# Kernel tuning notes

Hardware: AMD Instinct MI355X
Metric: run time of the kernel (lower is better)

Reference implementation:

```python
import jax, jax.numpy as jnp
import numpy as np

EPS = 1e-8  # matches TMLoss(eps=1e-08)


def setup_inputs() -> dict:
    key = jax.random.key(0)
    k1, k2 = jax.random.split(key)
    b, n = 2048, 1024
    # pseudo protein coords: spread out like real structures (~tens of Angstroms)
    pred = jax.random.normal(k1, (b, n, 3), dtype=jnp.float32) * 10.0
    # native coords = pred + noise, arbitrarily rotated/translated is fine since we Kabsch-align
    actual = pred + jax.random.normal(k2, (b, n, 3), dtype=jnp.float32)
    return {"predicted_coords": pred, "actual_coords": actual}


def _kabsch_align(align_to, align_from):
    """Rigidly align align_from onto align_to (batched Kabsch). Shapes (b,n,3)."""
    mu_to = jnp.mean(align_to, axis=1, keepdims=True)
    mu_from = jnp.mean(align_from, axis=1, keepdims=True)
    p = align_to - mu_to      # (b,n,3) target, centered
    q = align_from - mu_from  # (b,n,3) mobile, centered
    # 3x3 cross-covariance M = q^T p; optimal R maximizes tr(R^T M)
    M = jnp.einsum('bni,bnj->bij', q, p)  # (b,3,3)
    U, S, Vt = jnp.linalg.svd(M)
    # proper-rotation (det=+1) correction on smallest singular direction
    d = jnp.sign(jnp.linalg.det(U) * jnp.linalg.det(Vt))  # (b,)
    ones = jnp.ones_like(d)
    D = jnp.stack([ones, ones, d], axis=-1)               # (b,3)
    R = jnp.einsum('bik,bk,bkj->bij', U, D, Vt)           # (b,3,3)
    aligned = jnp.einsum('bni,bij->bnj', q, R) + mu_to    # (b,n,3)
    return align_to, aligned


def _calc_tm(dev, reduce=True):
    """dev: (b,n) per-residue deviations -> TM-score."""
    n = dev.shape[-1]
    d0 = 1.24 * (n - 15.0) ** (1.0 / 3.0) - 1.8
    tm = jnp.mean(1.0 / (1.0 + (dev / d0) ** 2), axis=-1)  # (b,)
    return jnp.mean(tm) if reduce else tm


def reference(predicted_coords, actual_coords):
    # align=True path: Kabsch-align native onto prediction
    _, aligned_actual = _kabsch_align(predicted_coords, actual_coords)
    # per-residue deviation (eps added elementwise before norm, as in torch source)
    dev = jnp.linalg.norm(predicted_coords - aligned_actual + EPS, axis=-1)  # (b,n)
    return -_calc_tm(dev, reduce=True)
```

## Files before the change

### kernel.cpp

```cpp
#include <hip/hip_runtime.h>
#include <math.h>

#define NRES 1024
#define TM_EPS 1e-8f

__global__ __launch_bounds__(256, 2) void tm_fused(const float* __restrict__ pred,
                                                   const float* __restrict__ act,
                                                   float* __restrict__ out,
                                                   float scale, float inv_d02) {
    __shared__ float4 sh[6][256];
    __shared__ float red[4][15];
    __shared__ float rotsh[12];

    int b = blockIdx.x;
    int t = threadIdx.x;
    const float4* p4 = (const float4*)(pred + (size_t)b * NRES * 3);
    const float4* a4 = (const float4*)(act  + (size_t)b * NRES * 3);

    float4 pf0 = p4[3 * t + 0], pf1 = p4[3 * t + 1], pf2 = p4[3 * t + 2];
    float4 af0 = a4[3 * t + 0], af1 = a4[3 * t + 1], af2 = a4[3 * t + 2];
    sh[0][t] = pf0; sh[1][t] = pf1; sh[2][t] = pf2;
    sh[3][t] = af0; sh[4][t] = af1; sh[5][t] = af2;

    {
        float px[4] = {pf0.x, pf0.w, pf1.z, pf2.y};
        float py[4] = {pf0.y, pf1.x, pf1.w, pf2.z};
        float pz[4] = {pf0.z, pf1.y, pf2.x, pf2.w};
        float ax[4] = {af0.x, af0.w, af1.z, af2.y};
        float ay[4] = {af0.y, af1.x, af1.w, af2.z};
        float az[4] = {af0.z, af1.y, af2.x, af2.w};

        float acc[15];
#pragma unroll
        for (int i = 0; i < 15; i++) acc[i] = 0.f;
#pragma unroll
        for (int r = 0; r < 4; r++) {
            acc[0] += px[r]; acc[1] += py[r]; acc[2] += pz[r];
            acc[3] += ax[r]; acc[4] += ay[r]; acc[5] += az[r];
            acc[6]  += ax[r] * px[r]; acc[7]  += ax[r] * py[r]; acc[8]  += ax[r] * pz[r];
            acc[9]  += ay[r] * px[r]; acc[10] += ay[r] * py[r]; acc[11] += ay[r] * pz[r];
            acc[12] += az[r] * px[r]; acc[13] += az[r] * py[r]; acc[14] += az[r] * pz[r];
        }
#pragma unroll
        for (int off = 32; off > 0; off >>= 1) {
#pragma unroll
            for (int i = 0; i < 15; i++) acc[i] += __shfl_down(acc[i], off);
        }
        int wave = t >> 6, lane = t & 63;
        if (lane == 0) {
#pragma unroll
            for (int i = 0; i < 15; i++) red[wave][i] = acc[i];
        }
    }
    __syncthreads();

    if (t == 0) {
        float s[15];
#pragma unroll
        for (int i = 0; i < 15; i++) s[i] = red[0][i] + red[1][i] + red[2][i] + red[3][i];

        const double n = (double)NRES;
        double mp[3], mq[3];
#pragma unroll
        for (int i = 0; i < 3; i++) { mp[i] = (double)s[i] / n; mq[i] = (double)s[3 + i] / n; }
        double M[3][3];
#pragma unroll
        for (int i = 0; i < 3; i++)
#pragma unroll
            for (int j = 0; j < 3; j++)
                M[i][j] = (double)s[6 + i * 3 + j] - n * mq[i] * mp[j];

        double Sxx = M[0][0], Sxy = M[0][1], Sxz = M[0][2];
        double Syx = M[1][0], Syy = M[1][1], Syz = M[1][2];
        double Szx = M[2][0], Szy = M[2][1], Szz = M[2][2];
        double K[4][4];
        K[0][0] = Sxx + Syy + Szz; K[0][1] = Syz - Szy;        K[0][2] = Szx - Sxz;         K[0][3] = Sxy - Syx;
        K[1][0] = K[0][1];         K[1][1] = Sxx - Syy - Szz;  K[1][2] = Sxy + Syx;         K[1][3] = Szx + Sxz;
        K[2][0] = K[0][2];         K[2][1] = K[1][2];          K[2][2] = -Sxx + Syy - Szz;  K[2][3] = Syz + Szy;
        K[3][0] = K[0][3];         K[3][1] = K[1][3];          K[3][2] = K[2][3];           K[3][3] = -Sxx - Syy + Szz;

        double K2[4][4];
#pragma unroll
        for (int i = 0; i < 4; i++)
#pragma unroll
            for (int j = 0; j < 4; j++) {
                double acc = 0.0;
#pragma unroll
                for (int k = 0; k < 4; k++) acc += K[i][k] * K[k][j];
                K2[i][j] = acc;
            }
        double p2 = 0.0, p3 = 0.0, p4s = 0.0;
#pragma unroll
        for (int i = 0; i < 4; i++)
#pragma unroll
            for (int j = 0; j < 4; j++) {
                p2 += K[i][j] * K[i][j];
                p3 += K2[i][j] * K[i][j];
                p4s += K2[i][j] * K2[i][j];
            }
        double e2 = -0.5 * p2;
        double e3 = p3 / 3.0;
        double e4 = (0.5 * p2 * p2 - p4s) * 0.25;

        double lam = sqrt(p2);
#pragma unroll
        for (int it = 0; it < 14; it++) {
            double lam2 = lam * lam;
            double P  = lam2 * lam2 + e2 * lam2 - e3 * lam + e4;
            double Pp = 4.0 * lam * lam2 + 2.0 * e2 * lam - e3;
            lam -= P / Pp;
        }

        double Bm[4][4];
#pragma unroll
        for (int i = 0; i < 4; i++)
#pragma unroll
            for (int j = 0; j < 4; j++) Bm[i][j] = K[i][j] - ((i == j) ? lam : 0.0);

        double cand[4][4];
#pragma unroll
        for (int r = 0; r < 4; r++) {
            int rr[3]; int k = 0;
#pragma unroll
            for (int i = 0; i < 4; i++) if (i != r) rr[k++] = i;
#pragma unroll
            for (int c = 0; c < 4; c++) {
                int cc[3]; int m = 0;
#pragma unroll
                for (int j = 0; j < 4; j++) if (j != c) cc[m++] = j;
                double d =
                    Bm[rr[0]][cc[0]] * (Bm[rr[1]][cc[1]] * Bm[rr[2]][cc[2]] - Bm[rr[1]][cc[2]] * Bm[rr[2]][cc[1]])
                  - Bm[rr[0]][cc[1]] * (Bm[rr[1]][cc[0]] * Bm[rr[2]][cc[2]] - Bm[rr[1]][cc[2]] * Bm[rr[2]][cc[0]])
                  + Bm[rr[0]][cc[2]] * (Bm[rr[1]][cc[0]] * Bm[rr[2]][cc[1]] - Bm[rr[1]][cc[1]] * Bm[rr[2]][cc[0]]);
                cand[r][c] = (((r + c) & 1) ? -d : d);
            }
        }
        int bestr = 0;
        double bestn = -1.0;
#pragma unroll
        for (int r = 0; r < 4; r++) {
            double nn = cand[r][0] * cand[r][0] + cand[r][1] * cand[r][1] +
                        cand[r][2] * cand[r][2] + cand[r][3] * cand[r][3];
            if (nn > bestn) { bestn = nn; bestr = r; }
        }
        double w = cand[bestr][0], x = cand[bestr][1], y = cand[bestr][2], z = cand[bestr][3];
        double nrm = sqrt(w * w + x * x + y * y + z * z);
        w /= nrm; x /= nrm; y /= nrm; z /= nrm;

        double A[3][3];
        A[0][0] = 1.0 - 2.0 * (y * y + z * z); A[0][1] = 2.0 * (x * y - w * z);       A[0][2] = 2.0 * (x * z + w * y);
        A[1][0] = 2.0 * (x * y + w * z);       A[1][1] = 1.0 - 2.0 * (x * x + z * z); A[1][2] = 2.0 * (y * z - w * x);
        A[2][0] = 2.0 * (x * z - w * y);       A[2][1] = 2.0 * (y * z + w * x);       A[2][2] = 1.0 - 2.0 * (x * x + y * y);

#pragma unroll
        for (int i = 0; i < 3; i++)
#pragma unroll
            for (int j = 0; j < 3; j++) rotsh[i * 3 + j] = (float)A[i][j];
#pragma unroll
        for (int i = 0; i < 3; i++)
            rotsh[9 + i] = (float)(mp[i] - (A[i][0] * mq[0] + A[i][1] * mq[1] + A[i][2] * mq[2]));
    }
    __syncthreads();

    float A00 = rotsh[0], A01 = rotsh[1], A02 = rotsh[2];
    float A10 = rotsh[3], A11 = rotsh[4], A12 = rotsh[5];
    float A20 = rotsh[6], A21 = rotsh[7], A22 = rotsh[8];
    float t0 = rotsh[9], t1 = rotsh[10], t2 = rotsh[11];

    float4 qf0 = sh[0][t], qf1 = sh[1][t], qf2 = sh[2][t];
    float4 bf0 = sh[3][t], bf1 = sh[4][t], bf2 = sh[5][t];

    float px[4] = {qf0.x, qf0.w, qf1.z, qf2.y};
    float py[4] = {qf0.y, qf1.x, qf1.w, qf2.z};
    float pz[4] = {qf0.z, qf1.y, qf2.x, qf2.w};
    float ax[4] = {bf0.x, bf0.w, bf1.z, bf2.y};
    float ay[4] = {bf0.y, bf1.x, bf1.w, bf2.z};
    float az[4] = {bf0.z, bf1.y, bf2.x, bf2.w};

    float sc = 0.f;
#pragma unroll
    for (int r = 0; r < 4; r++) {
        float dx = px[r] - (A00 * ax[r] + A01 * ay[r] + A02 * az[r]) - t0 + TM_EPS;
        float dy = py[r] - (A10 * ax[r] + A11 * ay[r] + A12 * az[r]) - t1 + TM_EPS;
        float dz = pz[r] - (A20 * ax[r] + A21 * ay[r] + A22 * az[r]) - t2 + TM_EPS;
        float d2 = dx * dx + dy * dy + dz * dz;
        sc += 1.0f / (1.0f + d2 * inv_d02);
    }
#pragma unroll
    for (int off = 32; off > 0; off >>= 1) sc += __shfl_down(sc, off);

    __shared__ float red2[4];
    int wave = t >> 6, lane = t & 63;
    if (lane == 0) red2[wave] = sc;
    __syncthreads();
    if (t == 0) {
        float tot = red2[0] + red2[1] + red2[2] + red2[3];
        atomicAdd(out, -tot * scale);
    }
}

extern "C" void kernel_launch(void* const* d_in, const int* in_sizes, int n_in,
                              void* d_out, int out_size, void* d_ws, size_t ws_size,
                              hipStream_t stream) {
    const float* pred = (const float*)d_in[0];
    const float* act  = (const float*)d_in[1];
    float* out = (float*)d_out;
    int B = in_sizes[0] / (NRES * 3);

    hipMemsetAsync(d_out, 0, sizeof(float), stream);

    double d0 = 1.24 * cbrt((double)NRES - 15.0) - 1.8;
    float inv_d02 = (float)(1.0 / (d0 * d0));
    float scale = 1.0f / ((float)B * (float)NRES);
    tm_fused<<<B, 256, 0, stream>>>(pred, act, out, scale, inv_d02);
}
```

Measured before the change: 110.1 us.

## Keep coordinates in registers and compute the rotation solve in fp32

Coordinates now stay in registers across the rotation solve instead of being staged through a 24KB shared-memory buffer. The single-thread quaternion eigen-solve switches from double to float, with two fewer Newton iterations and a reciprocal sqrt for normalisation. Launch bounds go from 2 to 4 blocks per SIMD to raise occupancy. This targets the serial fp64 tail run by thread 0 and the LDS limit on occupancy. The risks are fp32 accuracy loss in the covariance and eigenvalue steps and register pressure from holding 24 floats live across the solve.

After: 106.7 us. 3.0% less time.

```diff
diff --git a/kernel.cpp b/kernel.cpp
--- a/kernel.cpp
+++ b/kernel.cpp
@@ -4,13 +4,13 @@
 #define NRES 1024
 #define TM_EPS 1e-8f
 
-__global__ __launch_bounds__(256, 2) void tm_fused(const float* __restrict__ pred,
+__global__ __launch_bounds__(256, 4) void tm_fused(const float* __restrict__ pred,
                                                    const float* __restrict__ act,
                                                    float* __restrict__ out,
                                                    float scale, float inv_d02) {
-    __shared__ float4 sh[6][256];
     __shared__ float red[4][15];
     __shared__ float rotsh[12];
+    __shared__ float red2[4];
 
     int b = blockIdx.x;
     int t = threadIdx.x;
@@ -19,17 +19,15 @@
 
     float4 pf0 = p4[3 * t + 0], pf1 = p4[3 * t + 1], pf2 = p4[3 * t + 2];
     float4 af0 = a4[3 * t + 0], af1 = a4[3 * t + 1], af2 = a4[3 * t + 2];
-    sh[0][t] = pf0; sh[1][t] = pf1; sh[2][t] = pf2;
-    sh[3][t] = af0; sh[4][t] = af1; sh[5][t] = af2;
+
+    float px[4] = {pf0.x, pf0.w, pf1.z, pf2.y};
+    float py[4] = {pf0.y, pf1.x, pf1.w, pf2.z};
+    float pz[4] = {pf0.z, pf1.y, pf2.x, pf2.w};
+    float ax[4] = {af0.x, af0.w, af1.z, af2.y};
+    float ay[4] = {af0.y, af1.x, af1.w, af2.z};
+    float az[4] = {af0.z, af1.y, af2.x, af2.w};
 
     {
-        float px[4] = {pf0.x, pf0.w, pf1.z, pf2.y};
-        float py[4] = {pf0.y, pf1.x, pf1.w, pf2.z};
-        float pz[4] = {pf0.z, pf1.y, pf2.x, pf2.w};
-        float ax[4] = {af0.x, af0.w, af1.z, af2.y};
-        float ay[4] = {af0.y, af1.x, af1.w, af2.z};
-        float az[4] = {af0.z, af1.y, af2.x, af2.w};
-
         float acc[15];
 #pragma unroll
         for (int i = 0; i < 15; i++) acc[i] = 0.f;
@@ -59,37 +57,37 @@
 #pragma unroll
         for (int i = 0; i < 15; i++) s[i] = red[0][i] + red[1][i] + red[2][i] + red[3][i];
 
-        const double n = (double)NRES;
-        double mp[3], mq[3];
-#pragma unroll
-        for (int i = 0; i < 3; i++) { mp[i] = (double)s[i] / n; mq[i] = (double)s[3 + i] / n; }
-        double M[3][3];
+        const float n = (float)NRES;
+        float mp[3], mq[3];
+#pragma unroll
+        for (int i = 0; i < 3; i++) { mp[i] = s[i] / n; mq[i] = s[3 + i] / n; }
+        float M[3][3];
 #pragma unroll
         for (int i = 0; i < 3; i++)
 #pragma unroll
             for (int j = 0; j < 3; j++)
-                M[i][j] = (double)s[6 + i * 3 + j] - n * mq[i] * mp[j];
-
-        double Sxx = M[0][0], Sxy = M[0][1], Sxz = M[0][2];
-        double Syx = M[1][0], Syy = M[1][1], Syz = M[1][2];
-        double Szx = M[2][0], Szy = M[2][1], Szz = M[2][2];
-        double K[4][4];
+                M[i][j] = s[6 + i * 3 + j] - n * mq[i] * mp[j];
+
+        float Sxx = M[0][0], Sxy = M[0][1], Sxz = M[0][2];
+        float Syx = M[1][0], Syy = M[1][1], Syz = M[1][2];
+        float Szx = M[2][0], Szy = M[2][1], Szz = M[2][2];
+        float K[4][4];
         K[0][0] = Sxx + Syy + Szz; K[0][1] = Syz - Szy;        K[0][2] = Szx - Sxz;         K[0][3] = Sxy - Syx;
         K[1][0] = K[0][1];         K[1][1] = Sxx - Syy - Szz;  K[1][2] = Sxy + Syx;         K[1][3] = Szx + Sxz;
         K[2][0] = K[0][2];         K[2][1] = K[1][2];          K[2][2] = -Sxx + Syy - Szz;  K[2][3] = Syz + Szy;
         K[3][0] = K[0][3];         K[3][1] = K[1][3];          K[3][2] = K[2][3];           K[3][3] = -Sxx - Syy + Szz;
 
-        double K2[4][4];
+        float K2[4][4];
 #pragma unroll
         for (int i = 0; i < 4; i++)
 #pragma unroll
             for (int j = 0; j < 4; j++) {
-                double acc = 0.0;
+                float acc = 0.f;
 #pragma unroll
                 for (int k = 0; k < 4; k++) acc += K[i][k] * K[k][j];
                 K2[i][j] = acc;
             }
-        double p2 = 0.0, p3 = 0.0, p4s = 0.0;
+        float p2 = 0.f, p3 = 0.f, p4s = 0.f;
 #pragma unroll
         for (int i = 0; i < 4; i++)
 #pragma unroll
@@ -98,26 +96,26 @@
                 p3 += K2[i][j] * K[i][j];
                 p4s += K2[i][j] * K2[i][j];
             }
-        double e2 = -0.5 * p2;
-        double e3 = p3 / 3.0;
-        double e4 = (0.5 * p2 * p2 - p4s) * 0.25;
-
-        double lam = sqrt(p2);
-#pragma unroll
-        for (int it = 0; it < 14; it++) {
-            double lam2 = lam * lam;
-            double P  = lam2 * lam2 + e2 * lam2 - e3 * lam + e4;
-            double Pp = 4.0 * lam * lam2 + 2.0 * e2 * lam - e3;
+        float e2 = -0.5f * p2;
+        float e3 = p3 * (1.f / 3.f);
+        float e4 = (0.5f * p2 * p2 - p4s) * 0.25f;
+
+        float lam = sqrtf(p2);
+#pragma unroll
+        for (int it = 0; it < 12; it++) {
+            float lam2 = lam * lam;
+            float P  = lam2 * lam2 + e2 * lam2 - e3 * lam + e4;
+            float Pp = 4.f * lam * lam2 + 2.f * e2 * lam - e3;
             lam -= P / Pp;
         }
 
-        double Bm[4][4];
+        float Bm[4][4];
 #pragma unroll
         for (int i = 0; i < 4; i++)
 #pragma unroll
-            for (int j = 0; j < 4; j++) Bm[i][j] = K[i][j] - ((i == j) ? lam : 0.0);
-
-        double cand[4][4];
+            for (int j = 0; j < 4; j++) Bm[i][j] = K[i][j] - ((i == j) ? lam : 0.f);
+
+        float cand[4][4];
 #pragma unroll
         for (int r = 0; r < 4; r++) {
             int rr[3]; int k = 0;
@@ -128,7 +126,7 @@
                 int cc[3]; int m = 0;
 #pragma unroll
                 for (int j = 0; j < 4; j++) if (j != c) cc[m++] = j;
-                double d =
+                float d =
                     Bm[rr[0]][cc[0]] * (Bm[rr[1]][cc[1]] * Bm[rr[2]][cc[2]] - Bm[rr[1]][cc[2]] * Bm[rr[2]][cc[1]])
                   - Bm[rr[0]][cc[1]] * (Bm[rr[1]][cc[0]] * Bm[rr[2]][cc[2]] - Bm[rr[1]][cc[2]] * Bm[rr[2]][cc[0]])
                   + Bm[rr[0]][cc[2]] * (Bm[rr[1]][cc[0]] * Bm[rr[2]][cc[1]] - Bm[rr[1]][cc[1]] * Bm[rr[2]][cc[0]]);
@@ -136,29 +134,29 @@
             }
         }
         int bestr = 0;
-        double bestn = -1.0;
+        float bestn = -1.f;
 #pragma unroll
         for (int r = 0; r < 4; r++) {
-            double nn = cand[r][0] * cand[r][0] + cand[r][1] * cand[r][1] +
-                        cand[r][2] * cand[r][2] + cand[r][3] * cand[r][3];
+            float nn = cand[r][0] * cand[r][0] + cand[r][1] * cand[r][1] +
+                       cand[r][2] * cand[r][2] + cand[r][3] * cand[r][3];
             if (nn > bestn) { bestn = nn; bestr = r; }
         }
-        double w = cand[bestr][0], x = cand[bestr][1], y = cand[bestr][2], z = cand[bestr][3];
-        double nrm = sqrt(w * w + x * x + y * y + z * z);
-        w /= nrm; x /= nrm; y /= nrm; z /= nrm;
-
-        double A[3][3];
-        A[0][0] = 1.0 - 2.0 * (y * y + z * z); A[0][1] = 2.0 * (x * y - w * z);       A[0][2] = 2.0 * (x * z + w * y);
-        A[1][0] = 2.0 * (x * y + w * z);       A[1][1] = 1.0 - 2.0 * (x * x + z * z); A[1][2] = 2.0 * (y * z - w * x);
-        A[2][0] = 2.0 * (x * z - w * y);       A[2][1] = 2.0 * (y * z + w * x);       A[2][2] = 1.0 - 2.0 * (x * x + y * y);
+        float w = cand[bestr][0], x = cand[bestr][1], y = cand[bestr][2], z = cand[bestr][3];
+        float inrm = 1.f / sqrtf(w * w + x * x + y * y + z * z);
+        w *= inrm; x *= inrm; y *= inrm; z *= inrm;
+
+        float A[3][3];
+        A[0][0] = 1.f - 2.f * (y * y + z * z); A[0][1] = 2.f * (x * y - w * z);       A[0][2] = 2.f * (x * z + w * y);
+        A[1][0] = 2.f * (x * y + w * z);       A[1][1] = 1.f - 2.f * (x * x + z * z); A[1][2] = 2.f * (y * z - w * x);
+        A[2][0] = 2.f * (x * z - w * y);       A[2][1] = 2.f * (y * z + w * x);       A[2][2] = 1.f - 2.f * (x * x + y * y);
 
 #pragma unroll
         for (int i = 0; i < 3; i++)
 #pragma unroll
-            for (int j = 0; j < 3; j++) rotsh[i * 3 + j] = (float)A[i][j];
+            for (int j = 0; j < 3; j++) rotsh[i * 3 + j] = A[i][j];
 #pragma unroll
         for (int i = 0; i < 3; i++)
-            rotsh[9 + i] = (float)(mp[i] - (A[i][0] * mq[0] + A[i][1] * mq[1] + A[i][2] * mq[2]));
+            rotsh[9 + i] = mp[i] - (A[i][0] * mq[0] + A[i][1] * mq[1] + A[i][2] * mq[2]);
     }
     __syncthreads();
 
@@ -166,16 +164,6 @@
     float A10 = rotsh[3], A11 = rotsh[4], A12 = rotsh[5];
     float A20 = rotsh[6], A21 = rotsh[7], A22 = rotsh[8];
     float t0 = rotsh[9], t1 = rotsh[10], t2 = rotsh[11];
-
-    float4 qf0 = sh[0][t], qf1 = sh[1][t], qf2 = sh[2][t];
-    float4 bf0 = sh[3][t], bf1 = sh[4][t], bf2 = sh[5][t];
-
-    float px[4] = {qf0.x, qf0.w, qf1.z, qf2.y};
-    float py[4] = {qf0.y, qf1.x, qf1.w, qf2.z};
-    float pz[4] = {qf0.z, qf1.y, qf2.x, qf2.w};
-    float ax[4] = {bf0.x, bf0.w, bf1.z, bf2.y};
-    float ay[4] = {bf0.y, bf1.x, bf1.w, bf2.z};
-    float az[4] = {bf0.z, bf1.y, bf2.x, bf2.w};
 
     float sc = 0.f;
 #pragma unroll
@@ -189,7 +177,6 @@
 #pragma unroll
     for (int off = 32; off > 0; off >>= 1) sc += __shfl_down(sc, off);
 
-    __shared__ float red2[4];
     int wave = t >> 6, lane = t & 63;
     if (lane == 0) red2[wave] = sc;
     __syncthreads();
```
